# Optimization experiments

Hardware: AMD Instinct MI355X
Metric: run time of the kernel (lower is better)

## Reference

```python
import jax, jax.numpy as jnp
import numpy as np

# SMPL-like kinematic tree parents for 21 body joints (child j -> parent index in the 22-slot feature)
KTREE_PARENTS = jnp.array([0, 0, 0, 1, 2, 3, 4, 5, 6, 7, 8, 9, 9, 9, 12, 13, 14, 16, 17, 18, 19], dtype=jnp.int32)
# np.linspace(22, 64, 3, endpoint=False, dtype=int)[::-1] for num_tokens=64, token_size_div=3, num_joints+1=22
UP_SIZES = [50, 36, 22]
NUM_JOINTS_P1 = 22


def conv1d_rep(x, w, b):
    # x: (B, Cin, L), w: (Cout, Cin, 3), replicate padding of 1 on each side
    xp = jnp.pad(x, ((0, 0), (0, 0), (1, 1)), mode='edge')
    y = jax.lax.conv_general_dilated(xp, w, (1,), 'VALID', dimension_numbers=('NCH', 'OIH', 'NCH'))
    return y + b[None, :, None]


def interp_linear(x, out_size):
    # torch nn.Upsample(mode='linear', align_corners=False) semantics; x: (B, C, L)
    L = x.shape[-1]
    coords = (jnp.arange(out_size, dtype=x.dtype) + 0.5) * (L / out_size) - 0.5
    coords = jnp.clip(coords, 0.0, L - 1)
    lo = jnp.floor(coords).astype(jnp.int32)
    hi = jnp.minimum(lo + 1, L - 1)
    w = coords - lo.astype(x.dtype)
    return x[..., lo] * (1.0 - w) + x[..., hi] * w


def rotation_6d_to_matrix(d6):
    # pytorch3d convention: rows b1, b2, b3 stacked at dim=-2
    a1, a2 = d6[..., :3], d6[..., 3:]
    b1 = a1 / jnp.linalg.norm(a1, axis=-1, keepdims=True)
    a2p = a2 - jnp.sum(b1 * a2, axis=-1, keepdims=True) * b1
    b2 = a2p / jnp.linalg.norm(a2p, axis=-1, keepdims=True)
    b3 = jnp.cross(b1, b2)
    return jnp.stack([b1, b2, b3], axis=-2)


def setup_inputs() -> dict:
    key = jax.random.key(0)
    ks = jax.random.split(key, 8)
    B, T, C, W, J, D = 1024, 64, 512, 512, 21, 6
    s = 0.02
    f32 = jnp.float32
    return {
        'x': jax.random.normal(ks[0], (B, T, C), f32),
        'conv1_w': jax.random.normal(ks[1], (W, C, 3), f32) * s,
        'conv1_b': jnp.zeros((W,), f32),
        'tok_w': jax.random.normal(ks[2], (T, T), f32) * s,
        'tok_b': jnp.zeros((T,), f32),
        'up_w': jax.random.normal(ks[3], (3, W, W, 3), f32) * s,
        'up_b': jnp.zeros((3, W), f32),
        'ln_g': jnp.ones((W,), f32),
        'ln_b': jnp.zeros((W,), f32),
        'beta_w': jax.random.normal(ks[4], (W, 10), f32) * s,
        'beta_b': jnp.zeros((10,), f32),
        'pw1': jax.random.normal(ks[5], (J, 2 * W, W), f32) * s,
        'pb1': jnp.zeros((J, W), f32),
        'pw2': jax.random.normal(ks[6], (J, W, D), f32) * s,
        'pb2': jax.random.normal(ks[7], (J, D), f32) * 0.1,
    }


def reference(x, conv1_w, conv1_b, tok_w, tok_b, up_w, up_b, ln_g, ln_b,
              beta_w, beta_b, pw1, pb1, pw2, pb2):
    # ---- decoder ----
    h = x.transpose(0, 2, 1)                                   # (B, C, T)
    h = jax.nn.relu(conv1d_rep(h, conv1_w, conv1_b))            # (B, W, T)
    # Conv1d(T, T, 1) applied on token axis (after permutes) == matmul over tokens
    h = jax.nn.relu(jnp.einsum('st,bwt->bws', tok_w, h) + tok_b[None, None, :])  # (B, W, T)
    for i, sz in enumerate(UP_SIZES):
        h = conv1d_rep(interp_linear(h, sz), up_w[i], up_b[i])
        if sz != NUM_JOINTS_P1:
            h = jax.nn.relu(h)
    # h: (B, W, 22)
    m = h.mean(axis=-1)                                         # (B, W)
    mu = m.mean(-1, keepdims=True)
    var = m.var(-1, keepdims=True)
    pred_beta = ((m - mu) / jnp.sqrt(var + 1e-5) * ln_g + ln_b) @ beta_w + beta_b  # (B, 10)
    jf = h.transpose(0, 2, 1)                                   # (B, 22, W)
    curr = jf[:, 1:, :]                                         # joint j+1 feats, (B, 21, W)
    parent = jf[:, KTREE_PARENTS, :]                            # parent feats,   (B, 21, W)
    feat = jnp.concatenate([curr, parent], axis=-1)             # (B, 21, 2W)
    hid = jax.nn.relu(jnp.einsum('bjc,jch->bjh', feat, pw1) + pb1[None])
    pose6d = jnp.einsum('bjh,jhd->bjd', hid, pw2) + pb2[None]   # (B, 21, 6)
    rotmat = rotation_6d_to_matrix(pose6d)                      # (B, 21, 3, 3)
    return pose6d, rotmat, pred_beta
```

## Files before the change

### kernel.cpp

```cpp
#include <hip/hip_runtime.h>


typedef unsigned short u16;
typedef unsigned short u16x4 __attribute__((ext_vector_type(4)));
typedef unsigned short u16x8 __attribute__((ext_vector_type(8)));
typedef float f32x4 __attribute__((ext_vector_type(4)));
typedef __bf16 bf16x8 __attribute__((ext_vector_type(8)));

__constant__ int KPAR_C[21] = {0,0,0,1,2,3,4,5,6,7,8,9,9,9,12,13,14,16,17,18,19};

__device__ __forceinline__ u16 bf16rne(float v) {
  unsigned b = __builtin_bit_cast(unsigned, v);
  return (u16)((b + 0x7fffu + ((b >> 16) & 1u)) >> 16);
}
__device__ __forceinline__ float bf16tof(u16 h) {
  unsigned b = ((unsigned)h) << 16;
  return __builtin_bit_cast(float, b);
}
__device__ __forceinline__ f32x4 mfma16(u16x8 a, u16x8 b, f32x4 c) {
  return __builtin_amdgcn_mfma_f32_16x16x32_bf16(
      __builtin_bit_cast(bf16x8, a), __builtin_bit_cast(bf16x8, b), c, 0, 0, 0);
}

__global__ __launch_bounds__(256)
void kwprep(const float* __restrict__ conv1_w, const float* __restrict__ up_w,
            const float* __restrict__ tok_w, u16* __restrict__ WF, u16* __restrict__ TWF) {
  int idx = blockIdx.x * 256 + threadIdx.x;
  if (idx < 786432) {
    const int lane = idx & 63;
    int r = idx >> 6;
    const int nf = r & 15; r >>= 4;
    const int ks = r % 48; r /= 48;
    const int p = r & 1; r >>= 1;
    const int nh = r & 1;
    const int L = r >> 1;
    const float* Wsrc = (L == 0) ? conv1_w : (up_w + (size_t)(L - 1) * 786432);
    const int wcol = nh * 256 + nf * 16 + (lane & 15);
    u16x8 o;
#pragma unroll
    for (int e = 0; e < 8; ++e) {
      const int k = ks * 32 + ((lane >> 4) << 2) + (e & 3) + ((e >> 2) << 4);
      const int c = k & 511, kk = k >> 9;
      const float v = Wsrc[(size_t)wcol * 1536 + c * 3 + kk];
      const u16 h = bf16rne(v);
      o[e] = p ? bf16rne(v - bf16tof(h)) : h;
    }
    *(u16x8*)(WF + (size_t)idx * 8) = o;
  } else if (idx < 786432 + 1024) {
    const int i2 = idx - 786432;
    const int lane = i2 & 63;
    const int r = i2 >> 6;
    const int mf = r & 3;
    const int ks = (r >> 2) & 1;
    const int p = r >> 3;
    const int s = mf * 16 + (lane & 15);
    u16x8 o;
#pragma unroll
    for (int e = 0; e < 8; ++e) {
      const int t = ks * 32 + ((lane >> 4) << 2) + (e & 3) + ((e >> 2) << 4);
      const float v = tok_w[s * 64 + t];
      const u16 h = bf16rne(v);
      o[e] = p ? bf16rne(v - bf16tof(h)) : h;
    }
    *(u16x8*)(TWF + (size_t)i2 * 8) = o;
  }
}

__global__ __launch_bounds__(256)
void kpw1prep(const float* __restrict__ pw1, u16* __restrict__ PWF) {
  const int idx = blockIdx.x * 256 + threadIdx.x;
  if (idx >= 2752512) return;
  const int lane = idx & 63;
  const int nf = (idx >> 6) & 15;
  const int ks = (idx >> 10) & 31;
  const int p = (idx >> 15) & 1;
  const int nh = (idx >> 16) & 1;
  const int j = idx >> 17;
  const int w = nh * 256 + nf * 16 + (lane & 15);
  u16x8 o;
#pragma unroll
  for (int e = 0; e < 8; ++e) {
    const int k = ks * 32 + ((lane >> 4) << 2) + (e & 3) + ((e >> 2) << 4);
    const float v = pw1[((size_t)j * 1024 + k) * 512 + w];
    const u16 h = bf16rne(v);
    o[e] = p ? bf16rne(v - bf16tof(h)) : h;
  }
  *(u16x8*)(PWF + (size_t)idx * 8) = o;
}

template <int SLOT, int ROWS, bool SRCF32, bool F32OUT, bool RELU>
__global__ __launch_bounds__(512, 2)
void conv_gemm(const float* __restrict__ xf,
               const u16* __restrict__ ghi, const u16* __restrict__ glo,
               const u16* __restrict__ wl,
               const float* __restrict__ bias,
               u16* __restrict__ ohi, u16* __restrict__ olo,
               float* __restrict__ of32) {
  constexpr int MFW = SLOT / 16;
  constexpr int MFT = 4 * MFW;
  constexpr int ASL = (MFT + 7) / 8;
  __shared__ u16x8 Ald[2][2][MFT][64];
  __shared__ u16x8 Bld[2][2][16][64];

  const int tid = threadIdx.x, lane = tid & 63, w = tid >> 6;
  const int mw = w & 3, nw = w >> 2;
  const int nh = blockIdx.x;
  const int bb0 = blockIdx.y * 4;

  f32x4 acc[MFW][8];
#pragma unroll
  for (int m = 0; m < MFW; ++m)
#pragma unroll
    for (int n = 0; n < 8; ++n) acc[m][n] = (f32x4){0.f, 0.f, 0.f, 0.f};

  float4 sF[ASL][2];
  u16x8 sH[ASL], sL[ASL];
  u16x8 sB[4];

  auto LOADS = [&](int ks2) {
    const int kk2 = ks2 >> 4;
    const int c0 = (ks2 & 15) * 32 + ((lane >> 4) << 2);
#pragma unroll
    for (int si = 0; si < ASL; ++si) {
      const int f = w + si * 8;
      if (f < MFT) {
        const int bA = f / MFW, mfA = f % MFW;
        int t = mfA * 16 + (lane & 15) - 1 + kk2;
        t = t < 0 ? 0 : (t > ROWS - 1 ? ROWS - 1 : t);
        const size_t o = ((size_t)(bb0 + bA) * ROWS + t) * 512 + c0;
        if constexpr (SRCF32) {
          sF[si][0] = *(const float4*)(xf + o);
          sF[si][1] = *(const float4*)(xf + o + 16);
        } else {
          const u16x4 a = *(const u16x4*)(ghi + o);
          const u16x4 b = *(const u16x4*)(ghi + o + 16);
          const u16x4 c = *(const u16x4*)(glo + o);
          const u16x4 d = *(const u16x4*)(glo + o + 16);
          sH[si] = (u16x8){a[0], a[1], a[2], a[3], b[0], b[1], b[2], b[3]};
          sL[si] = (u16x8){c[0], c[1], c[2], c[3], d[0], d[1], d[2], d[3]};
        }
      }
    }
#pragma unroll
    for (int ci = 0; ci < 4; ++ci) {
      const int cch = w + ci * 8;
      const int p = cch >> 4, nf = cch & 15;
      sB[ci] = *(const u16x8*)(wl + ((size_t)(((nh * 2 + p) * 48 + ks2) * 16 + nf)) * 512 + lane * 8);
    }
  };

  auto WRITES = [&](int nb) {
#pragma unroll
    for (int si = 0; si < ASL; ++si) {
      const int f = w + si * 8;
      if (f < MFT) {
        u16x8 hv, lv;
        if constexpr (SRCF32) {
          float vv[8] = {sF[si][0].x, sF[si][0].y, sF[si][0].z, sF[si][0].w,
                         sF[si][1].x, sF[si][1].y, sF[si][1].z, sF[si][1].w};
#pragma unroll
          for (int e = 0; e < 8; ++e) {
            const u16 h = bf16rne(vv[e]);
            hv[e] = h;
            lv[e] = bf16rne(vv[e] - bf16tof(h));
          }
        } else {
          hv = sH[si];
          lv = sL[si];
        }
        Ald[nb][0][f][lane] = hv;
        Ald[nb][1][f][lane] = lv;
      }
    }
#pragma unroll
    for (int ci = 0; ci < 4; ++ci) {
      const int cch = w + ci * 8;
      Bld[nb][cch >> 4][cch & 15][lane] = sB[ci];
    }
  };

  LOADS(0);
  WRITES(0);
  __syncthreads();

  for (int ks = 0; ks < 48; ++ks) {
    const int buf = ks & 1;
    if (ks < 47) LOADS(ks + 1);
    u16x8 ah[MFW], al[MFW];
#pragma unroll
    for (int m = 0; m < MFW; ++m) {
      ah[m] = Ald[buf][0][mw * MFW + m][lane];
      al[m] = Ald[buf][1][mw * MFW + m][lane];
    }
#pragma unroll
    for (int n = 0; n < 8; ++n) {
      const u16x8 bh = Bld[buf][0][nw * 8 + n][lane];
      const u16x8 bl = Bld[buf][1][nw * 8 + n][lane];
#pragma unroll
      for (int m = 0; m < MFW; ++m) {
        acc[m][n] = mfma16(ah[m], bh, acc[m][n]);
        acc[m][n] = mfma16(ah[m], bl, acc[m][n]);
        acc[m][n] = mfma16(al[m], bh, acc[m][n]);
      }
    }
    if (ks < 47) WRITES(buf ^ 1);
    __syncthreads();
  }

  const int b = bb0 + mw;
#pragma unroll
  for (int m = 0; m < MFW; ++m) {
#pragma unroll
    for (int n = 0; n < 8; ++n) {
      const int col = nh * 256 + nw * 128 + n * 16 + (lane & 15);
      const float bs = bias[col];
#pragma unroll
      for (int r = 0; r < 4; ++r) {
        const int t = m * 16 + ((lane >> 4) << 2) + r;
        if (t < ROWS) {
          float v = acc[m][n][r] + bs;
          if (RELU) v = fmaxf(v, 0.f);
          const size_t o = ((size_t)b * ROWS + t) * 512 + col;
          if constexpr (F32OUT) {
            of32[o] = v;
          } else {
            const u16 h = bf16rne(v);
            ohi[o] = h;
            olo[o] = bf16rne(v - bf16tof(h));
          }
        }
      }
    }
  }
}

__global__ __launch_bounds__(512, 2)
void tok_mix(const u16* __restrict__ h1hi, const u16* __restrict__ h1lo,
             const u16* __restrict__ twf, const float* __restrict__ tok_b,
             u16* __restrict__ g1hi, u16* __restrict__ g1lo) {
  __shared__ float h1f[64][258];
  __shared__ u16x8 twl[2][2][4][64];
  __shared__ float tbl[64];
  const int tid = threadIdx.x, lane = tid & 63, w = tid >> 6;
  const int mw = w & 3, nw = w >> 2;
  const int b = blockIdx.y, ch = blockIdx.x;

  for (int i = tid; i < 1024; i += 512) ((u16x8*)twl)[i] = ((const u16x8*)twf)[i];
  if (tid < 64) tbl[tid] = tok_b[tid];
  for (int i = tid; i < 2048; i += 512) {
    const int t = i >> 5, c8 = (i & 31) * 8;
    const size_t o = ((size_t)b * 64 + t) * 512 + ch * 256 + c8;
    const u16x8 hv = *(const u16x8*)(h1hi + o);
    const u16x8 lv = *(const u16x8*)(h1lo + o);
#pragma unroll
    for (int e = 0; e < 8; ++e) h1f[t][c8 + e] = bf16tof(hv[e]) + bf16tof(lv[e]);
  }
  __syncthreads();

  f32x4 acc2[8];
#pragma unroll
  for (int n = 0; n < 8; ++n) acc2[n] = (f32x4){0.f, 0.f, 0.f, 0.f};
#pragma unroll
  for (int ksI = 0; ksI < 2; ++ksI) {
    const u16x8 ah = twl[0][ksI][mw][lane];
    const u16x8 al = twl[1][ksI][mw][lane];
    const int t0 = ksI * 32 + ((lane >> 4) << 2);
#pragma unroll
    for (int n = 0; n < 8; ++n) {
      const int c = nw * 128 + n * 16 + (lane & 15);
      u16x8 bh, bl;
#pragma unroll
      for (int e = 0; e < 8; ++e) {
        const float v = h1f[t0 + (e & 3) + ((e >> 2) << 4)][c];
        const u16 h = bf16rne(v);
        bh[e] = h;
        bl[e] = bf16rne(v - bf16tof(h));
      }
      acc2[n] = mfma16(ah, bh, acc2[n]);
      acc2[n] = mfma16(ah, bl, acc2[n]);
      acc2[n] = mfma16(al, bh, acc2[n]);
    }
  }
  __syncthreads();
#pragma unroll
  for (int n = 0; n < 8; ++n) {
    const int c = nw * 128 + n * 16 + (lane & 15);
#pragma unroll
    for (int r = 0; r < 4; ++r) {
      const int s = mw * 16 + ((lane >> 4) << 2) + r;
      h1f[s][c] = fmaxf(acc2[n][r] + tbl[s], 0.f);
    }
  }
  __syncthreads();
  const float scale = (float)(64.0 / 50.0);
  for (int i = tid; i < 50 * 256; i += 512) {
    const int s = i >> 8, c = i & 255;
    float coords = fminf(fmaxf(((float)s + 0.5f) * scale - 0.5f, 0.f), 63.f);
    const int lo = (int)floorf(coords);
    const int hi = lo + 1 < 64 ? lo + 1 : 63;
    const float wv = coords - (float)lo;
    const float v = h1f[lo][c] * (1.f - wv) + h1f[hi][c] * wv;
    const u16 h = bf16rne(v);
    const size_t o = ((size_t)b * 50 + s) * 512 + ch * 256 + c;
    g1hi[o] = h;
    g1lo[o] = bf16rne(v - bf16tof(h));
  }
}

template <int SOUT, int SIN>
__global__ __launch_bounds__(256)
void ginterp(const u16* __restrict__ ahi, const u16* __restrict__ alo,
             u16* __restrict__ ghi, u16* __restrict__ glo) {
  const int idx = blockIdx.x * 256 + threadIdx.x;
  if (idx >= 1024 * SOUT * 64) return;
  const int ch = (idx & 63) * 8;
  const int s = (idx >> 6) % SOUT;
  const int b = (idx >> 6) / SOUT;
  const float scale = (float)((double)SIN / (double)SOUT);
  float coords = fminf(fmaxf(((float)s + 0.5f) * scale - 0.5f, 0.f), (float)(SIN - 1));
  const int lo = (int)floorf(coords);
  const int hi = lo + 1 < SIN ? lo + 1 : SIN - 1;
  const float wv = coords - (float)lo;
  const size_t olo_ = ((size_t)b * SIN + lo) * 512 + ch;
  const size_t ohi_ = ((size_t)b * SIN + hi) * 512 + ch;
  const u16x8 vh0 = *(const u16x8*)(ahi + olo_), vl0 = *(const u16x8*)(alo + olo_);
  const u16x8 vh1 = *(const u16x8*)(ahi + ohi_), vl1 = *(const u16x8*)(alo + ohi_);
  u16x8 oh, ol;
#pragma unroll
  for (int e = 0; e < 8; ++e) {
    const float v0 = bf16tof(vh0[e]) + bf16tof(vl0[e]);
    const float v1 = bf16tof(vh1[e]) + bf16tof(vl1[e]);
    const float v = v0 * (1.f - wv) + v1 * wv;
    const u16 h = bf16rne(v);
    oh[e] = h;
    ol[e] = bf16rne(v - bf16tof(h));
  }
  const size_t oo = ((size_t)b * SOUT + s) * 512 + ch;
  *(u16x8*)(ghi + oo) = oh;
  *(u16x8*)(glo + oo) = ol;
}

__global__ __launch_bounds__(256)
void k_beta(const float* __restrict__ h, const float* __restrict__ ln_g,
            const float* __restrict__ ln_b, const float* __restrict__ beta_w,
            const float* __restrict__ beta_b, float* __restrict__ out) {
  __shared__ float nbuf[512];
  __shared__ float red[32];
  __shared__ float part[160];
  const int tid = threadIdx.x;
  const int b = blockIdx.x;
  const float* hb = h + (size_t)b * (22 * 512);
  float m0 = 0.f, m1 = 0.f;
  for (int t = 0; t < 22; ++t) {
    m0 += hb[t * 512 + tid];
    m1 += hb[t * 512 + tid + 256];
  }
  m0 *= (1.f / 22.f);
  m1 *= (1.f / 22.f);
  float s = m0 + m1, sq = m0 * m0 + m1 * m1;
  for (int off = 32; off > 0; off >>= 1) {
    s += __shfl_down(s, off);
    sq += __shfl_down(sq, off);
  }
  const int lane = tid & 63, wid = tid >> 6;
  if (lane == 0) { red[wid] = s; red[8 + wid] = sq; }
  __syncthreads();
  if (tid == 0) {
    float S = red[0] + red[1] + red[2] + red[3];
    float Q = red[8] + red[9] + red[10] + red[11];
    float mu = S * (1.f / 512.f);
    float var = Q * (1.f / 512.f) - mu * mu;
    red[16] = mu;
    red[17] = 1.f / sqrtf(var + 1e-5f);
  }
  __syncthreads();
  const float mu = red[16], rs = red[17];
  nbuf[tid] = (m0 - mu) * rs * ln_g[tid] + ln_b[tid];
  nbuf[tid + 256] = (m1 - mu) * rs * ln_g[tid + 256] + ln_b[tid + 256];
  __syncthreads();
  if (tid < 160) {
    const int o = tid >> 4, l = tid & 15;
    float p = 0.f;
    for (int w = l; w < 512; w += 16) p += nbuf[w] * beta_w[w * 10 + o];
    part[tid] = p;
  }
  __syncthreads();
  if (tid < 10) {
    float p = beta_b[tid];
#pragma unroll
    for (int l = 0; l < 16; ++l) p += part[tid * 16 + l];
    out[(size_t)b * 10 + tid] = p;
  }
}

__global__ __launch_bounds__(512, 2)
void k_pose1(const float* __restrict__ hf, const u16* __restrict__ PWF,
             const float* __restrict__ pb1,
             u16* __restrict__ hidhi, u16* __restrict__ hidlo) {
  __shared__ u16x8 Ald[2][2][8][64];
  __shared__ u16x8 Bld[2][2][16][64];
  const int tid = threadIdx.x, lane = tid & 63, w = tid >> 6;
  const int mw = w & 1, nw = w >> 1;
  const int nh = blockIdx.x & 1, mb = blockIdx.x >> 1;
  const int j = blockIdx.y;
  const int bb0 = mb * 128;
  const int par = KPAR_C[j];
  const size_t pwbase = (size_t)(j * 2 + nh) * 524288;

  f32x4 acc[4][4];
#pragma unroll
  for (int m = 0; m < 4; ++m)
#pragma unroll
    for (int n = 0; n < 4; ++n) acc[m][n] = (f32x4){0.f, 0.f, 0.f, 0.f};

  float4 sF0, sF1;
  u16x8 sB[4];

  auto LOADS = [&](int ks) {
    const int row = (ks < 16) ? (j + 1) : par;
    const int b = bb0 + w * 16 + (lane & 15);
    const int c0 = (ks & 15) * 32 + ((lane >> 4) << 2);
    const float* src = hf + ((size_t)b * 22 + row) * 512 + c0;
    sF0 = *(const float4*)src;
    sF1 = *(const float4*)(src + 16);
#pragma unroll
    for (int t = 0; t < 4; ++t) {
      const int cc = t * 8 + w;
      const int p = cc >> 4, nf = cc & 15;
      sB[t] = *(const u16x8*)(PWF + pwbase + ((size_t)(p * 32 + ks) * 16 + nf) * 512 + lane * 8);
    }
  };
  auto WRITES = [&](int nb) {
    float vv[8] = {sF0.x, sF0.y, sF0.z, sF0.w, sF1.x, sF1.y, sF1.z, sF1.w};
    u16x8 hv, lv;
#pragma unroll
    for (int e = 0; e < 8; ++e) {
      const u16 h = bf16rne(vv[e]);
      hv[e] = h;
      lv[e] = bf16rne(vv[e] - bf16tof(h));
    }
    Ald[nb][0][w][lane] = hv;
    Ald[nb][1][w][lane] = lv;
#pragma unroll
    for (int t = 0; t < 4; ++t) {
      const int cc = t * 8 + w;
      Bld[nb][cc >> 4][cc & 15][lane] = sB[t];
    }
  };

  LOADS(0);
  WRITES(0);
  __syncthreads();

  for (int ks = 0; ks < 32; ++ks) {
    const int buf = ks & 1;
    if (ks < 31) LOADS(ks + 1);
    u16x8 ah[4], al[4], bh[4], bl[4];
#pragma unroll
    for (int m = 0; m < 4; ++m) {
      ah[m] = Ald[buf][0][mw * 4 + m][lane];
      al[m] = Ald[buf][1][mw * 4 + m][lane];
    }
#pragma unroll
    for (int n = 0; n < 4; ++n) {
      bh[n] = Bld[buf][0][nw * 4 + n][lane];
      bl[n] = Bld[buf][1][nw * 4 + n][lane];
    }
#pragma unroll
    for (int n = 0; n < 4; ++n)
#pragma unroll
      for (int m = 0; m < 4; ++m) {
        acc[m][n] = mfma16(ah[m], bh[n], acc[m][n]);
        acc[m][n] = mfma16(ah[m], bl[n], acc[m][n]);
        acc[m][n] = mfma16(al[m], bh[n], acc[m][n]);
      }
    if (ks < 31) WRITES(buf ^ 1);
    __syncthreads();
  }

#pragma unroll
  for (int m = 0; m < 4; ++m) {
#pragma unroll
    for (int n = 0; n < 4; ++n) {
      const int col = nh * 256 + nw * 64 + n * 16 + (lane & 15);
      const float bs = pb1[(size_t)j * 512 + col];
#pragma unroll
      for (int r = 0; r < 4; ++r) {
        const int b = bb0 + mw * 64 + m * 16 + ((lane >> 4) << 2) + r;
        float v = fmaxf(acc[m][n][r] + bs, 0.f);
        const size_t o = ((size_t)j * 1024 + b) * 512 + col;
        const u16 h = bf16rne(v);
        hidhi[o] = h;
        hidlo[o] = bf16rne(v - bf16tof(h));
      }
    }
  }
}

__global__ __launch_bounds__(256)
void k_pose2(const u16* __restrict__ hidhi, const u16* __restrict__ hidlo,
             const float* __restrict__ pw2, const float* __restrict__ pb2,
             float* __restrict__ out) {
  __shared__ float w2l[3072];
  __shared__ float part[128 * 12];
  const int tid = threadIdx.x;
  const int mb = blockIdx.x, j = blockIdx.y;
  const int bb0 = mb * 128;
  for (int i = tid; i < 3072; i += 256) w2l[i] = pw2[(size_t)j * 3072 + i];
  __syncthreads();

  const int r = tid >> 1, half = tid & 1;
  const int row = bb0 + r;
  const u16* ph = hidhi + ((size_t)j * 1024 + row) * 512 + half * 256;
  const u16* pl = hidlo + ((size_t)j * 1024 + row) * 512 + half * 256;
  float s[6] = {0.f, 0.f, 0.f, 0.f, 0.f, 0.f};
  for (int c = 0; c < 32; ++c) {
    const u16x8 hv = ((const u16x8*)ph)[c];
    const u16x8 lv = ((const u16x8*)pl)[c];
#pragma unroll
    for (int e = 0; e < 8; ++e) {
      const float v = bf16tof(hv[e]) + bf16tof(lv[e]);
      const int hidx = half * 256 + c * 8 + e;
#pragma unroll
      for (int d = 0; d < 6; ++d) s[d] = fmaf(v, w2l[hidx * 6 + d], s[d]);
    }
  }
#pragma unroll
  for (int d = 0; d < 6; ++d) part[r * 12 + half * 6 + d] = s[d];
  __syncthreads();

  if (tid < 128) {
    const int row2 = bb0 + tid;
    float p6[6];
#pragma unroll
    for (int d = 0; d < 6; ++d)
      p6[d] = part[tid * 12 + d] + part[tid * 12 + 6 + d] + pb2[j * 6 + d];
    float* po = out + ((size_t)row2 * 21 + j) * 6;
#pragma unroll
    for (int d = 0; d < 6; ++d) po[d] = p6[d];
    const float a1x = p6[0], a1y = p6[1], a1z = p6[2];
    const float a2x = p6[3], a2y = p6[4], a2z = p6[5];
    const float inv1 = 1.f / sqrtf(a1x * a1x + a1y * a1y + a1z * a1z);
    const float b1x = a1x * inv1, b1y = a1y * inv1, b1z = a1z * inv1;
    const float dot = b1x * a2x + b1y * a2y + b1z * a2z;
    const float px = a2x - dot * b1x, py = a2y - dot * b1y, pz = a2z - dot * b1z;
    const float inv2 = 1.f / sqrtf(px * px + py * py + pz * pz);
    const float b2x = px * inv2, b2y = py * inv2, b2z = pz * inv2;
    const float b3x = b1y * b2z - b1z * b2y;
    const float b3y = b1z * b2x - b1x * b2z;
    const float b3z = b1x * b2y - b1y * b2x;
    float* ro = out + 129024 + ((size_t)row2 * 21 + j) * 9;
    ro[0] = b1x; ro[1] = b1y; ro[2] = b1z;
    ro[3] = b2x; ro[4] = b2y; ro[5] = b2z;
    ro[6] = b3x; ro[7] = b3y; ro[8] = b3z;
  }
}

extern "C" void kernel_launch(void* const* d_in, const int* in_sizes, int n_in,
                              void* d_out, int out_size, void* d_ws, size_t ws_size,
                              hipStream_t stream) {
  (void)in_sizes; (void)n_in; (void)out_size; (void)ws_size;
  const float* x       = (const float*)d_in[0];
  const float* conv1_w = (const float*)d_in[1];
  const float* conv1_b = (const float*)d_in[2];
  const float* tok_w   = (const float*)d_in[3];
  const float* tok_b   = (const float*)d_in[4];
  const float* up_w    = (const float*)d_in[5];
  const float* up_b    = (const float*)d_in[6];
  const float* ln_g    = (const float*)d_in[7];
  const float* ln_b    = (const float*)d_in[8];
  const float* beta_w  = (const float*)d_in[9];
  const float* beta_b  = (const float*)d_in[10];
  const float* pw1     = (const float*)d_in[11];
  const float* pb1     = (const float*)d_in[12];
  const float* pw2     = (const float*)d_in[13];
  const float* pb2     = (const float*)d_in[14];
  float* outp = (float*)d_out;

  char* base = (char*)d_ws;
  u16* WF  = (u16*)base;
  u16* TWF = WF + 6291456;
  u16* PA16 = (u16*)(base + 12599296);
  u16* PB16 = (u16*)(base + 12599296 + 134217728);
  u16* h1hi = PA16;            u16* h1lo = PA16 + 33554432;
  u16* a2hi = PA16;            u16* a2lo = PA16 + 26214400;
  u16* a3hi = PA16;            u16* a3lo = PA16 + 18874368;
  float* hf = (float*)PA16;
  u16* g1hi = PB16;            u16* g1lo = PB16 + 26214400;
  u16* g2hi = PB16;            u16* g2lo = PB16 + 18874368;
  u16* g3hi = PB16;            u16* g3lo = PB16 + 11534336;
  u16* PWF   = PB16;
  u16* hidhi = PB16 + 22020096;
  u16* hidlo = PB16 + 33030144;

  const size_t WL = 1572864;

  kwprep<<<3076, 256, 0, stream>>>(conv1_w, up_w, tok_w, WF, TWF);
  conv_gemm<64, 64, true, false, true><<<dim3(2, 256), 512, 0, stream>>>(
      x, nullptr, nullptr, WF, conv1_b, h1hi, h1lo, nullptr);
  tok_mix<<<dim3(2, 1024), 512, 0, stream>>>(h1hi, h1lo, TWF, tok_b, g1hi, g1lo);
  conv_gemm<64, 50, false, false, true><<<dim3(2, 256), 512, 0, stream>>>(
      nullptr, g1hi, g1lo, WF + WL, up_b, a2hi, a2lo, nullptr);
  ginterp<36, 50><<<9216, 256, 0, stream>>>(a2hi, a2lo, g2hi, g2lo);
  conv_gemm<48, 36, false, false, true><<<dim3(2, 256), 512, 0, stream>>>(
      nullptr, g2hi, g2lo, WF + 2 * WL, up_b + 512, a3hi, a3lo, nullptr);
  ginterp<22, 36><<<5632, 256, 0, stream>>>(a3hi, a3lo, g3hi, g3lo);
  conv_gemm<32, 22, false, true, false><<<dim3(2, 256), 512, 0, stream>>>(
      nullptr, g3hi, g3lo, WF + 3 * WL, up_b + 1024, nullptr, nullptr, hf);
  kpw1prep<<<10752, 256, 0, stream>>>(pw1, PWF);
  k_pose1<<<dim3(16, 21), 512, 0, stream>>>(hf, PWF, pb1, hidhi, hidlo);
  k_beta<<<1024, 256, 0, stream>>>(hf, ln_g, ln_b, beta_w, beta_b, outp + 322560);
  k_pose2<<<dim3(8, 21), 256, 0, stream>>>(hidhi, hidlo, pw2, pb2, outp);
}
```

Baseline: 1.253 ms.

## Stage GEMM operands via direct global-to-LDS loads with permuted channel layout

The conv and pose1 GEMM kernels now load weight tiles, and bf16 hi/lo activation tiles where they are already bf16, straight into LDS with global_load_lds. This replaces the register round-trip and the separate LDS write step. To make contiguous 16-byte loads line up with the MFMA fragment order, the channel dimension is stored in a permuted order (unpack_c), and the weight prep, bias, layernorm, beta and pose2 indexing are remapped to match. It also raises wave priority around the MFMA loop with s_setprio. The risk is that the permutation must be consistent across every consumer, and the async LDS loads now depend on the existing barrier for ordering.

Result: slower. 1.363 ms (+8.7%).

```diff
diff --git a/kernel.cpp b/kernel.cpp
--- a/kernel.cpp
+++ b/kernel.cpp
@@ -20,6 +20,13 @@
 __device__ __forceinline__ f32x4 mfma16(u16x8 a, u16x8 b, f32x4 c) {
   return __builtin_amdgcn_mfma_f32_16x16x32_bf16(
       __builtin_bit_cast(bf16x8, a), __builtin_bit_cast(bf16x8, b), c, 0, 0, 0);
+}
+__device__ __forceinline__ int unpack_c(int p) {
+  return (p & ~31) | (((p >> 3) & 3) << 2) | (p & 3) | ((p & 4) << 2);
+}
+__device__ __forceinline__ void gload_lds16(const void* g, void* l) {
+  __builtin_amdgcn_global_load_lds((const __attribute__((address_space(1))) void*)g,
+                                   (__attribute__((address_space(3))) void*)l, 16, 0, 0);
 }
 
 __global__ __launch_bounds__(256)
@@ -35,7 +42,7 @@
     const int nh = r & 1;
     const int L = r >> 1;
     const float* Wsrc = (L == 0) ? conv1_w : (up_w + (size_t)(L - 1) * 786432);
-    const int wcol = nh * 256 + nf * 16 + (lane & 15);
+    const int wcol = unpack_c(nh * 256 + nf * 16 + (lane & 15));
     u16x8 o;
 #pragma unroll
     for (int e = 0; e < 8; ++e) {
@@ -76,7 +83,7 @@
   const int p = (idx >> 15) & 1;
   const int nh = (idx >> 16) & 1;
   const int j = idx >> 17;
-  const int w = nh * 256 + nf * 16 + (lane & 15);
+  const int w = unpack_c(nh * 256 + nf * 16 + (lane & 15));
   u16x8 o;
 #pragma unroll
   for (int e = 0; e < 8; ++e) {
@@ -113,11 +120,35 @@
 #pragma unroll
     for (int n = 0; n < 8; ++n) acc[m][n] = (f32x4){0.f, 0.f, 0.f, 0.f};
 
-  float4 sF[ASL][2];
-  u16x8 sH[ASL], sL[ASL];
-  u16x8 sB[4];
-
-  auto LOADS = [&](int ks2) {
+  float4 sF0[ASL], sF1[ASL];
+
+  auto STAGE = [&](int ks2, int nb) {
+    if constexpr (!SRCF32) {
+      const int kk2 = ks2 >> 4;
+      const int pc0 = (ks2 & 15) * 32 + ((lane >> 4) << 3);
+#pragma unroll
+      for (int si = 0; si < ASL; ++si) {
+        const int f = w + si * 8;
+        if (f < MFT) {
+          const int bA = f / MFW, mfA = f % MFW;
+          int t = mfA * 16 + (lane & 15) - 1 + kk2;
+          t = t < 0 ? 0 : (t > ROWS - 1 ? ROWS - 1 : t);
+          const size_t o = ((size_t)(bb0 + bA) * ROWS + t) * 512 + pc0;
+          gload_lds16(ghi + o, &Ald[nb][0][f][0]);
+          gload_lds16(glo + o, &Ald[nb][1][f][0]);
+        }
+      }
+    }
+#pragma unroll
+    for (int ci = 0; ci < 4; ++ci) {
+      const int cch = w + ci * 8;
+      const int p = cch >> 4, nf = cch & 15;
+      gload_lds16(wl + ((size_t)(((nh * 2 + p) * 48 + ks2) * 16 + nf)) * 512 + lane * 8,
+                  &Bld[nb][p][nf][0]);
+    }
+  };
+
+  auto LOADSA = [&](int ks2) {
     const int kk2 = ks2 >> 4;
     const int c0 = (ks2 & 15) * 32 + ((lane >> 4) << 2);
 #pragma unroll
@@ -127,71 +158,49 @@
         const int bA = f / MFW, mfA = f % MFW;
         int t = mfA * 16 + (lane & 15) - 1 + kk2;
         t = t < 0 ? 0 : (t > ROWS - 1 ? ROWS - 1 : t);
-        const size_t o = ((size_t)(bb0 + bA) * ROWS + t) * 512 + c0;
-        if constexpr (SRCF32) {
-          sF[si][0] = *(const float4*)(xf + o);
-          sF[si][1] = *(const float4*)(xf + o + 16);
-        } else {
-          const u16x4 a = *(const u16x4*)(ghi + o);
-          const u16x4 b = *(const u16x4*)(ghi + o + 16);
-          const u16x4 c = *(const u16x4*)(glo + o);
-          const u16x4 d = *(const u16x4*)(glo + o + 16);
-          sH[si] = (u16x8){a[0], a[1], a[2], a[3], b[0], b[1], b[2], b[3]};
-          sL[si] = (u16x8){c[0], c[1], c[2], c[3], d[0], d[1], d[2], d[3]};
-        }
-      }
-    }
-#pragma unroll
-    for (int ci = 0; ci < 4; ++ci) {
-      const int cch = w + ci * 8;
-      const int p = cch >> 4, nf = cch & 15;
-      sB[ci] = *(const u16x8*)(wl + ((size_t)(((nh * 2 + p) * 48 + ks2) * 16 + nf)) * 512 + lane * 8);
+        const float* src = xf + ((size_t)(bb0 + bA) * ROWS + t) * 512 + c0;
+        sF0[si] = *(const float4*)src;
+        sF1[si] = *(const float4*)(src + 16);
+      }
     }
   };
-
-  auto WRITES = [&](int nb) {
+  auto WRITESA = [&](int nb) {
 #pragma unroll
     for (int si = 0; si < ASL; ++si) {
       const int f = w + si * 8;
       if (f < MFT) {
+        float vv[8] = {sF0[si].x, sF0[si].y, sF0[si].z, sF0[si].w,
+                       sF1[si].x, sF1[si].y, sF1[si].z, sF1[si].w};
         u16x8 hv, lv;
-        if constexpr (SRCF32) {
-          float vv[8] = {sF[si][0].x, sF[si][0].y, sF[si][0].z, sF[si][0].w,
-                         sF[si][1].x, sF[si][1].y, sF[si][1].z, sF[si][1].w};
-#pragma unroll
-          for (int e = 0; e < 8; ++e) {
-            const u16 h = bf16rne(vv[e]);
-            hv[e] = h;
-            lv[e] = bf16rne(vv[e] - bf16tof(h));
-          }
-        } else {
-          hv = sH[si];
-          lv = sL[si];
+#pragma unroll
+        for (int e = 0; e < 8; ++e) {
+          const u16 h = bf16rne(vv[e]);
+          hv[e] = h;
+          lv[e] = bf16rne(vv[e] - bf16tof(h));
         }
         Ald[nb][0][f][lane] = hv;
         Ald[nb][1][f][lane] = lv;
       }
     }
-#pragma unroll
-    for (int ci = 0; ci < 4; ++ci) {
-      const int cch = w + ci * 8;
-      Bld[nb][cch >> 4][cch & 15][lane] = sB[ci];
-    }
   };
 
-  LOADS(0);
-  WRITES(0);
+  STAGE(0, 0);
+  if constexpr (SRCF32) { LOADSA(0); WRITESA(0); }
   __syncthreads();
 
   for (int ks = 0; ks < 48; ++ks) {
     const int buf = ks & 1;
-    if (ks < 47) LOADS(ks + 1);
+    if (ks < 47) {
+      STAGE(ks + 1, buf ^ 1);
+      if constexpr (SRCF32) LOADSA(ks + 1);
+    }
     u16x8 ah[MFW], al[MFW];
 #pragma unroll
     for (int m = 0; m < MFW; ++m) {
       ah[m] = Ald[buf][0][mw * MFW + m][lane];
       al[m] = Ald[buf][1][mw * MFW + m][lane];
     }
+    __builtin_amdgcn_s_setprio(1);
 #pragma unroll
     for (int n = 0; n < 8; ++n) {
       const u16x8 bh = Bld[buf][0][nw * 8 + n][lane];
@@ -203,7 +212,10 @@
         acc[m][n] = mfma16(al[m], bh, acc[m][n]);
       }
     }
-    if (ks < 47) WRITES(buf ^ 1);
+    __builtin_amdgcn_s_setprio(0);
+    if (ks < 47) {
+      if constexpr (SRCF32) WRITESA(buf ^ 1);
+    }
     __syncthreads();
   }
 
@@ -213,7 +225,7 @@
 #pragma unroll
     for (int n = 0; n < 8; ++n) {
       const int col = nh * 256 + nw * 128 + n * 16 + (lane & 15);
-      const float bs = bias[col];
+      const float bs = bias[unpack_c(col)];
 #pragma unroll
       for (int r = 0; r < 4; ++r) {
         const int t = m * 16 + ((lane >> 4) << 2) + r;
@@ -375,13 +387,14 @@
   }
   __syncthreads();
   const float mu = red[16], rs = red[17];
-  nbuf[tid] = (m0 - mu) * rs * ln_g[tid] + ln_b[tid];
-  nbuf[tid + 256] = (m1 - mu) * rs * ln_g[tid + 256] + ln_b[tid + 256];
+  const int uc = unpack_c(tid);
+  nbuf[tid] = (m0 - mu) * rs * ln_g[uc] + ln_b[uc];
+  nbuf[tid + 256] = (m1 - mu) * rs * ln_g[uc + 256] + ln_b[uc + 256];
   __syncthreads();
   if (tid < 160) {
     const int o = tid >> 4, l = tid & 15;
     float p = 0.f;
-    for (int w = l; w < 512; w += 16) p += nbuf[w] * beta_w[w * 10 + o];
+    for (int w = l; w < 512; w += 16) p += nbuf[w] * beta_w[unpack_c(w) * 10 + o];
     part[tid] = p;
   }
   __syncthreads();
@@ -414,23 +427,25 @@
     for (int n = 0; n < 4; ++n) acc[m][n] = (f32x4){0.f, 0.f, 0.f, 0.f};
 
   float4 sF0, sF1;
-  u16x8 sB[4];
-
-  auto LOADS = [&](int ks) {
-    const int row = (ks < 16) ? (j + 1) : par;
-    const int b = bb0 + w * 16 + (lane & 15);
-    const int c0 = (ks & 15) * 32 + ((lane >> 4) << 2);
-    const float* src = hf + ((size_t)b * 22 + row) * 512 + c0;
-    sF0 = *(const float4*)src;
-    sF1 = *(const float4*)(src + 16);
+
+  auto STAGE = [&](int ks, int nb) {
 #pragma unroll
     for (int t = 0; t < 4; ++t) {
       const int cc = t * 8 + w;
       const int p = cc >> 4, nf = cc & 15;
-      sB[t] = *(const u16x8*)(PWF + pwbase + ((size_t)(p * 32 + ks) * 16 + nf) * 512 + lane * 8);
+      gload_lds16(PWF + pwbase + ((size_t)(p * 32 + ks) * 16 + nf) * 512 + lane * 8,
+                  &Bld[nb][p][nf][0]);
     }
   };
-  auto WRITES = [&](int nb) {
+  auto LOADSA = [&](int ks) {
+    const int row = (ks < 16) ? (j + 1) : par;
+    const int b = bb0 + w * 16 + (lane & 15);
+    const int pc0 = (ks & 15) * 32 + ((lane >> 4) << 3);
+    const float* src = hf + ((size_t)b * 22 + row) * 512 + pc0;
+    sF0 = *(const float4*)src;
+    sF1 = *(const float4*)(src + 4);
+  };
+  auto WRITESA = [&](int nb) {
     float vv[8] = {sF0.x, sF0.y, sF0.z, sF0.w, sF1.x, sF1.y, sF1.z, sF1.w};
     u16x8 hv, lv;
 #pragma unroll
@@ -441,20 +456,16 @@
     }
     Ald[nb][0][w][lane] = hv;
     Ald[nb][1][w][lane] = lv;
-#pragma unroll
-    for (int t = 0; t < 4; ++t) {
-      const int cc = t * 8 + w;
-      Bld[nb][cc >> 4][cc & 15][lane] = sB[t];
-    }
   };
 
-  LOADS(0);
-  WRITES(0);
+  STAGE(0, 0);
+  LOADSA(0);
+  WRITESA(0);
   __syncthreads();
 
   for (int ks = 0; ks < 32; ++ks) {
     const int buf = ks & 1;
-    if (ks < 31) LOADS(ks + 1);
+    if (ks < 31) { STAGE(ks + 1, buf ^ 1); LOADSA(ks + 1); }
     u16x8 ah[4], al[4], bh[4], bl[4];
 #pragma unroll
     for (int m = 0; m < 4; ++m) {
@@ -466,6 +477,7 @@
       bh[n] = Bld[buf][0][nw * 4 + n][lane];
       bl[n] = Bld[buf][1][nw * 4 + n][lane];
     }
+    __builtin_amdgcn_s_setprio(1);
 #pragma unroll
     for (int n = 0; n < 4; ++n)
 #pragma unroll
@@ -474,7 +486,8 @@
         acc[m][n] = mfma16(ah[m], bl[n], acc[m][n]);
         acc[m][n] = mfma16(al[m], bh[n], acc[m][n]);
       }
-    if (ks < 31) WRITES(buf ^ 1);
+    __builtin_amdgcn_s_setprio(0);
+    if (ks < 31) WRITESA(buf ^ 1);
     __syncthreads();
   }
 
@@ -483,7 +496,7 @@
 #pragma unroll
     for (int n = 0; n < 4; ++n) {
       const int col = nh * 256 + nw * 64 + n * 16 + (lane & 15);
-      const float bs = pb1[(size_t)j * 512 + col];
+      const float bs = pb1[(size_t)j * 512 + unpack_c(col)];
 #pragma unroll
       for (int r = 0; r < 4; ++r) {
         const int b = bb0 + mw * 64 + m * 16 + ((lane >> 4) << 2) + r;
@@ -506,7 +519,10 @@
   const int tid = threadIdx.x;
   const int mb = blockIdx.x, j = blockIdx.y;
   const int bb0 = mb * 128;
-  for (int i = tid; i < 3072; i += 256) w2l[i] = pw2[(size_t)j * 3072 + i];
+  for (int i = tid; i < 3072; i += 256) {
+    const int p = i / 6, d = i - p * 6;
+    w2l[i] = pw2[(size_t)j * 3072 + unpack_c(p) * 6 + d];
+  }
   __syncthreads();
 
   const int r = tid >> 1, half = tid & 1;
```
